# Performance work log

Measured on AMD Instinct MI355X. Metric: run time of the kernel, lower is better.

## Reference

```python
import jax, jax.numpy as jnp
import numpy as np

NEG_SLOPE = 0.01  # torch F.leaky_relu default

def _lrelu(x):
    return jax.nn.leaky_relu(x, NEG_SLOPE)

def setup_inputs() -> dict:
    key = jax.random.key(0)
    ks = jax.random.split(key, 24)
    B, N, E = 512, 20000, 640000
    n_enc_1, n_enc_2, n_z = 512, 256, 64
    n_dec_2, n_dec_1, hidden = 256, 512, 256
    p = lambda k, shp, fan: jax.random.normal(k, shp, jnp.float32) * (1.0 / np.sqrt(fan))
    return {
        "data": jax.random.normal(ks[0], (B, N), jnp.float32),
        "noise": jax.random.normal(ks[1], (B, N), jnp.float32),
        "edge_index": jax.random.randint(ks[2], (2, E), 0, N, jnp.int32),
        "w_gcn": jax.random.normal(ks[3], (), jnp.float32),
        "b_gcn": jax.random.normal(ks[4], (), jnp.float32) * 0.1,
        "enc1_w": p(ks[5], (N, n_enc_1), N), "enc1_b": p(ks[6], (n_enc_1,), N),
        "enc2_w": p(ks[7], (n_enc_1, n_enc_2), n_enc_1), "enc2_b": p(ks[8], (n_enc_2,), n_enc_1),
        "enc3_w": p(ks[9], (n_enc_2, n_z), n_enc_2), "enc3_b": p(ks[10], (n_z,), n_enc_2),
        "dec1_w": p(ks[11], (n_z, n_dec_2), n_z), "dec1_b": p(ks[12], (n_dec_2,), n_z),
        "dec2_w": p(ks[13], (n_dec_2, n_dec_1), n_dec_2), "dec2_b": p(ks[14], (n_dec_1,), n_dec_2),
        "dec3_w": p(ks[15], (n_dec_1, N), n_dec_1), "dec3_b": p(ks[16], (N,), n_dec_1),
        "disc1_w": p(ks[17], (n_z, hidden), n_z), "disc1_b": p(ks[18], (hidden,), n_z),
        "disc2_w": p(ks[19], (hidden, hidden), hidden), "disc2_b": p(ks[20], (hidden,), hidden),
        "disc3_w": p(ks[21], (hidden, 1), hidden), "disc3_b": p(ks[22], (1,), hidden),
    }

def _gcn_batched(x, edge_index, w_gcn, b_gcn):
    # x: [B, N] -> GCNConv(1,1, improved=True) applied per row, vectorized.
    B, N = x.shape
    src, dst = edge_index[0], edge_index[1]
    loop = jnp.arange(N, dtype=src.dtype)
    src_a = jnp.concatenate([src, loop])
    dst_a = jnp.concatenate([dst, loop])
    # improved=True: self-loop edge weight 2.0
    ew = jnp.concatenate([jnp.ones(src.shape[0], x.dtype), jnp.full((N,), 2.0, x.dtype)])
    deg = jax.ops.segment_sum(ew, dst_a, num_segments=N)
    dinv = jnp.where(deg > 0, jax.lax.rsqrt(deg), 0.0)
    norm = dinv[src_a] * ew * dinv[dst_a]  # [E+N]
    xl = x * w_gcn                         # lin (1x1 weight, no bias)
    msgs = xl[:, src_a] * norm[None, :]    # [B, E+N]
    agg = jnp.zeros_like(x).at[:, dst_a].add(msgs)
    return agg + b_gcn

def reference(data, noise, edge_index, w_gcn, b_gcn,
              enc1_w, enc1_b, enc2_w, enc2_b, enc3_w, enc3_b,
              dec1_w, dec1_b, dec2_w, dec2_b, dec3_w, dec3_b,
              disc1_w, disc1_b, disc2_w, disc2_b, disc3_w, disc3_b):
    x = data + noise * 0.1
    gcn_out = _lrelu(_gcn_batched(x, edge_index, w_gcn, b_gcn))  # [B, N]
    h1 = _lrelu(gcn_out @ enc1_w + enc1_b)
    h2 = _lrelu(h1 @ enc2_w + enc2_b)
    z = _lrelu(h2 @ enc3_w + enc3_b)
    d1 = _lrelu(z @ dec1_w + dec1_b)
    d2 = _lrelu(d1 @ dec2_w + dec2_b)
    dec_h3 = _lrelu(d2 @ dec3_w + dec3_b)
    g1 = _lrelu(z @ disc1_w + disc1_b)
    g2 = _lrelu(g1 @ disc2_w + disc2_b)
    d = jax.nn.sigmoid(g2 @ disc3_w + disc3_b)
    return (dec_h3, z, d)
```

## Files before the change

### kernel.cpp

```cpp
#include <hip/hip_runtime.h>
#include <hip/hip_bf16.h>


#define LRELU(v) ((v) > 0.f ? (v) : 0.01f * (v))

static constexpr int Bb = 512;
static constexpr int Nn = 20000;
static constexpr int Ee = 640000;
static constexpr int KPAD = 20480;
static constexpr int RSU = 36;
static constexpr int RSW = 18;

typedef __attribute__((ext_vector_type(8))) short short8;
typedef __attribute__((ext_vector_type(4))) short short4v;
typedef __attribute__((ext_vector_type(4))) float f32x4;

__device__ __forceinline__ ushort f2bf(float f) {
  uint u = __builtin_bit_cast(uint, f);
  u = u + 0x7FFFu + ((u >> 16) & 1u);
  return (ushort)(u >> 16);
}
__device__ __forceinline__ float bfLo(uint u) {
  return __builtin_bit_cast(float, u << 16);
}
__device__ __forceinline__ float bfHi(uint u) {
  return __builtin_bit_cast(float, u & 0xffff0000u);
}

__global__ void transpose_xs_k(const float* __restrict__ a, const float* __restrict__ nz,
                               const float* __restrict__ dinv, ushort* __restrict__ xs, int b0) {
  __shared__ ushort tile[64][65];
  int c0 = blockIdx.x * 64;
  int p = blockIdx.y;
  int chunk = p >> 1;
  int sub = (p & 1) * 64;
  int rbase = b0 + p * 64;
  for (int i = threadIdx.x; i < 64 * 64; i += 256) {
    int rr = i >> 6, cc = i & 63;
    int r = rbase + rr, c = c0 + cc;
    ushort v = 0;
    if (c < Nn) {
      size_t idx = (size_t)r * Nn + c;
      v = f2bf(dinv[c] * (a[idx] + 0.1f * nz[idx]));
    }
    tile[rr][cc] = v;
  }
  __syncthreads();
  for (int i = threadIdx.x; i < 64 * 64; i += 256) {
    int cc = i >> 6, rr = i & 63;
    int c = c0 + cc;
    if (c < Nn) xs[(size_t)chunk * Nn * 128 + (size_t)c * 128 + sub + rr] = tile[rr][cc];
  }
}

__global__ void hist_check_k(const int* __restrict__ src, const int* __restrict__ dst, int E,
                             int* __restrict__ cnt, int* __restrict__ flag) {
  int i = blockIdx.x * 256 + threadIdx.x;
  if (i < E) {
    int s = src[i], d = dst[i];
    if ((unsigned)s >= (unsigned)Nn || (unsigned)d >= (unsigned)Nn) {
      atomicExch(flag, 1);
    } else {
      atomicAdd(&cnt[d], 1);
    }
  }
}

__global__ void offs_k(const int* __restrict__ cnt, int* __restrict__ offs,
                       int* __restrict__ cursor, float* __restrict__ dinv,
                       int* __restrict__ bump) {
  int i = blockIdx.x * 256 + threadIdx.x;
  int l = threadIdx.x & 63;
  int v = (i < Nn) ? cnt[i] : 0;
  int x = v;
#pragma unroll
  for (int d = 1; d < 64; d <<= 1) {
    int t = __shfl_up(x, d);
    if (l >= d) x += t;
  }
  int total = __shfl(x, 63);
  int base = 0;
  if (l == 0) base = atomicAdd(bump, total);
  base = __shfl(base, 0);
  int excl = base + x - v;
  if (i < Nn) {
    offs[i] = excl;
    cursor[i] = excl;
    dinv[i] = rsqrtf(2.0f + (float)v);
  }
}

__global__ void scatter_k(const int* __restrict__ src, const int* __restrict__ dst, int E,
                          int* __restrict__ cursor, uint* __restrict__ eOff) {
  int i = blockIdx.x * 256 + threadIdx.x;
  if (i < E) {
    int s = src[i], d = dst[i];
    if ((unsigned)s >= (unsigned)Nn || (unsigned)d >= (unsigned)Nn) return;
    int p = atomicAdd(&cursor[d], 1);
    eOff[p] = (uint)s * 256u;
  }
}

__global__ __launch_bounds__(256) void spmm_chunk_k(
    const ushort* __restrict__ xs, const uint* __restrict__ eOff, const int* __restrict__ offs,
    const int* __restrict__ cnt, const float* __restrict__ dinv, const float* __restrict__ wg,
    const float* __restrict__ bg, ushort* __restrict__ gcnT, int NC) {
  __shared__ uint sIdx[4][64];
  int bid = blockIdx.x;
  int chunk = bid % NC;
  int ngrp = bid / NC;
  int wv = threadIdx.x >> 6, l = threadIdx.x & 63;
  int n = ngrp * 4 + wv;
  int o = offs[n], c = cnt[n];
  const char* base = (const char*)(xs + (size_t)chunk * Nn * 128) + l * 4;
  const uint* ep = eOff + o;
  uint su = *(const uint*)(base + (size_t)n * 256);
  float a00 = 2.0f * bfLo(su), a01 = 2.0f * bfHi(su);
  float a10 = 0.f, a11 = 0.f;

  for (int bi = 0; bi < c; bi += 64) {
    int rem = c - bi;
    if (rem > 64) rem = 64;
    sIdx[wv][l] = (l < rem) ? ep[bi + l] : 0u;
    int i = 0;
    for (; i + 8 <= rem; i += 8) {
      uint u[8];
#pragma unroll
      for (int j = 0; j < 8; ++j) u[j] = *(const uint*)(base + sIdx[wv][i + j]);
#pragma unroll
      for (int j = 0; j < 8; j += 2) {
        a00 += bfLo(u[j]);
        a01 += bfHi(u[j]);
        a10 += bfLo(u[j + 1]);
        a11 += bfHi(u[j + 1]);
      }
    }
    for (; i < rem; ++i) {
      uint u = *(const uint*)(base + sIdx[wv][i]);
      a00 += bfLo(u);
      a01 += bfHi(u);
    }
  }

  float wdn = wg[0] * dinv[n], bb = bg[0];
  float v0 = wdn * (a00 + a10) + bb;
  float v1 = wdn * (a01 + a11) + bb;
  v0 = LRELU(v0);
  v1 = LRELU(v1);
  uint pk = (uint)f2bf(v0) | ((uint)f2bf(v1) << 16);
  *(uint*)&gcnT[(size_t)chunk * KPAD * 128 + (size_t)n * 128 + 2 * l] = pk;
}

template <bool SPLITK>
__global__ __launch_bounds__(256) void mfma_gemm3(const ushort* __restrict__ AT, int lda, int pw,
                                                  size_t pstride, const float* __restrict__ B,
                                                  int ldb, int KB, int Nv, int iters,
                                                  float* __restrict__ C, int ldc,
                                                  const float* __restrict__ bias) {
  __shared__ ushort As[128 * RSU];
  __shared__ ushort Bs[128 * RSU];
  int n0 = blockIdx.x * 128, m0 = blockIdx.y * 128;
  int k0 = blockIdx.z * iters * 32;
  int tid = threadIdx.x;
  int kp = tid >> 4;
  int c8 = (tid & 15) * 8;
  int l = tid & 63, w = tid >> 6;
  int wr = w >> 1, wc = w & 1;
  int lrow = l & 15, lkg = l >> 4;
  const ushort* Ap = AT + (size_t)(m0 / pw) * pstride + (m0 % pw);
  int bcol = n0 + c8;
  bool bok = bcol < Nv;
  f32x4 acc[4][4] = {};

  uint4 pa0, pa1;
  float4 pb00, pb01, pb10, pb11;

#define GLOAD(KG)                                                                       \
  {                                                                                     \
    int kq = (KG) + 2 * kp;                                                             \
    pa0 = *(const uint4*)&Ap[(size_t)kq * lda + c8];                                    \
    pa1 = *(const uint4*)&Ap[(size_t)(kq + 1) * lda + c8];                              \
    pb00 = pb01 = pb10 = pb11 = float4{0.f, 0.f, 0.f, 0.f};                             \
    if (bok) {                                                                          \
      if (kq < KB) {                                                                    \
        const float4* bp = (const float4*)(B + (size_t)kq * ldb + bcol);                \
        pb00 = bp[0];                                                                   \
        pb01 = bp[1];                                                                   \
      }                                                                                 \
      if (kq + 1 < KB) {                                                                \
        const float4* bp = (const float4*)(B + (size_t)(kq + 1) * ldb + bcol);          \
        pb10 = bp[0];                                                                   \
        pb11 = bp[1];                                                                   \
      }                                                                                 \
    }                                                                                   \
  }

  GLOAD(k0);

  for (int kt = 0; kt < iters; ++kt) {
    uint wa[8], wb[8];
    wa[0] = (pa0.x & 0xffffu) | (pa1.x << 16);
    wa[1] = (pa0.x >> 16) | (pa1.x & 0xffff0000u);
    wa[2] = (pa0.y & 0xffffu) | (pa1.y << 16);
    wa[3] = (pa0.y >> 16) | (pa1.y & 0xffff0000u);
    wa[4] = (pa0.z & 0xffffu) | (pa1.z << 16);
    wa[5] = (pa0.z >> 16) | (pa1.z & 0xffff0000u);
    wa[6] = (pa0.w & 0xffffu) | (pa1.w << 16);
    wa[7] = (pa0.w >> 16) | (pa1.w & 0xffff0000u);
    wb[0] = (uint)f2bf(pb00.x) | ((uint)f2bf(pb10.x) << 16);
    wb[1] = (uint)f2bf(pb00.y) | ((uint)f2bf(pb10.y) << 16);
    wb[2] = (uint)f2bf(pb00.z) | ((uint)f2bf(pb10.z) << 16);
    wb[3] = (uint)f2bf(pb00.w) | ((uint)f2bf(pb10.w) << 16);
    wb[4] = (uint)f2bf(pb01.x) | ((uint)f2bf(pb11.x) << 16);
    wb[5] = (uint)f2bf(pb01.y) | ((uint)f2bf(pb11.y) << 16);
    wb[6] = (uint)f2bf(pb01.z) | ((uint)f2bf(pb11.z) << 16);
    wb[7] = (uint)f2bf(pb01.w) | ((uint)f2bf(pb11.w) << 16);
    __syncthreads();
    {
      uint* aw = (uint*)As;
      uint* bw = (uint*)Bs;
#pragma unroll
      for (int j = 0; j < 8; ++j) {
        aw[(c8 + j) * RSW + kp] = wa[j];
        bw[(c8 + j) * RSW + kp] = wb[j];
      }
    }
    __syncthreads();
    if (kt + 1 < iters) GLOAD(k0 + (kt + 1) * 32);
    short8 a[4], b[4];
#pragma unroll
    for (int mi = 0; mi < 4; ++mi) {
      int m = wr * 64 + mi * 16 + lrow;
      const short4v* p = (const short4v*)&As[m * RSU + lkg * 8];
      a[mi] = __builtin_shufflevector(p[0], p[1], 0, 1, 2, 3, 4, 5, 6, 7);
    }
#pragma unroll
    for (int nj = 0; nj < 4; ++nj) {
      int n = wc * 64 + nj * 16 + lrow;
      const short4v* p = (const short4v*)&Bs[n * RSU + lkg * 8];
      b[nj] = __builtin_shufflevector(p[0], p[1], 0, 1, 2, 3, 4, 5, 6, 7);
    }
#pragma unroll
    for (int mi = 0; mi < 4; ++mi)
#pragma unroll
      for (int nj = 0; nj < 4; ++nj)
        acc[mi][nj] = __builtin_amdgcn_mfma_f32_16x16x32_bf16(a[mi], b[nj], acc[mi][nj], 0, 0, 0);
  }
#undef GLOAD

#pragma unroll
  for (int mi = 0; mi < 4; ++mi)
#pragma unroll
    for (int nj = 0; nj < 4; ++nj)
#pragma unroll
      for (int r = 0; r < 4; ++r) {
        int row = m0 + wr * 64 + mi * 16 + lkg * 4 + r;
        int col = n0 + wc * 64 + nj * 16 + lrow;
        if (SPLITK) {
          atomicAdd(&C[(size_t)row * ldc + col], acc[mi][nj][r]);
        } else if (col < Nv) {
          float v = acc[mi][nj][r] + bias[col];
          C[(size_t)row * ldc + col] = LRELU(v);
        }
      }
}

__global__ __launch_bounds__(256) void tail2_k(
    const float* __restrict__ h1, const float* __restrict__ c1, const float* __restrict__ W2,
    const float* __restrict__ c2, const float* __restrict__ W3, const float* __restrict__ c3,
    const float* __restrict__ Wd1, const float* __restrict__ cd1, const float* __restrict__ Wd2,
    const float* __restrict__ cd2, const float* __restrict__ Wg1, const float* __restrict__ cg1,
    const float* __restrict__ Wg2, const float* __restrict__ cg2, const float* __restrict__ Wg3,
    const float* __restrict__ cg3, float* __restrict__ out_z, float* __restrict__ out_d,
    ushort* __restrict__ d2bfT, int BT, int b0) {
  __shared__ float s_h1[512];
  __shared__ float s_h2[256];
  __shared__ float s_z[64];
  __shared__ float s_d1[256];
  __shared__ float s_g1[256];
  __shared__ float s_g2[256];
  __shared__ float s_part[4][256];
  __shared__ float s_red[4];
  int rl = blockIdx.x;
  int rg = b0 + rl;
  int t = threadIdx.x;
  int w = t >> 6, l = t & 63;

  {
    float r0 = h1[(size_t)rl * 512 + t] + c1[t];
    float r1 = h1[(size_t)rl * 512 + t + 256] + c1[t + 256];
    s_h1[t] = LRELU(r0);
    s_h1[t + 256] = LRELU(r1);
  }
  __syncthreads();

  {
    int c4 = l * 4;
    float a0 = 0.f, a1 = 0.f, a2 = 0.f, a3 = 0.f;
#pragma unroll 8
    for (int k = w * 128; k < w * 128 + 128; ++k) {
      float4 wv = *(const float4*)&W2[(size_t)k * 256 + c4];
      float x = s_h1[k];
      a0 += x * wv.x; a1 += x * wv.y; a2 += x * wv.z; a3 += x * wv.w;
    }
    float4 pv = {a0, a1, a2, a3};
    *(float4*)&s_part[w][c4] = pv;
  }
  __syncthreads();
  s_h2[t] = LRELU(s_part[0][t] + s_part[1][t] + s_part[2][t] + s_part[3][t] + c2[t]);
  __syncthreads();

  {
    int c = t >> 2, p = t & 3;
    float a = 0.f;
#pragma unroll 8
    for (int k = p * 64; k < p * 64 + 64; ++k) a += s_h2[k] * W3[(size_t)k * 64 + c];
    s_part[p][c] = a;
  }
  __syncthreads();
  if (t < 64) {
    float v = s_part[0][t] + s_part[1][t] + s_part[2][t] + s_part[3][t] + c3[t];
    v = LRELU(v);
    s_z[t] = v;
    out_z[(size_t)rg * 64 + t] = v;
  }
  __syncthreads();

  {
    float a = 0.f;
#pragma unroll
    for (int k = 0; k < 64; ++k) a += s_z[k] * Wd1[(size_t)k * 256 + t];
    s_d1[t] = LRELU(a + cd1[t]);
  }
  {
    float a = 0.f;
#pragma unroll
    for (int k = 0; k < 64; ++k) a += s_z[k] * Wg1[(size_t)k * 256 + t];
    s_g1[t] = LRELU(a + cg1[t]);
  }
  __syncthreads();

  {
    int g = t & 127, p = t >> 7;
    int c4 = g * 4;
    float a0 = 0.f, a1 = 0.f, a2 = 0.f, a3 = 0.f;
#pragma unroll 8
    for (int k = p * 128; k < p * 128 + 128; ++k) {
      float4 wv = *(const float4*)&Wd2[(size_t)k * 512 + c4];
      float x = s_d1[k];
      a0 += x * wv.x; a1 += x * wv.y; a2 += x * wv.z; a3 += x * wv.w;
    }
    float* sp = &s_part[0][0];
    float4 pv = {a0, a1, a2, a3};
    *(float4*)&sp[p * 512 + c4] = pv;
  }
  __syncthreads();
  {
    const float* sp = &s_part[0][0];
#pragma unroll
    for (int cc = 0; cc < 2; ++cc) {
      int c = t + cc * 256;
      float v = sp[c] + sp[512 + c] + cd2[c];
      v = LRELU(v);
      d2bfT[(size_t)c * BT + rl] = f2bf(v);
    }
  }
  __syncthreads();

  {
    int c4 = l * 4;
    float a0 = 0.f, a1 = 0.f, a2 = 0.f, a3 = 0.f;
#pragma unroll 8
    for (int k = w * 64; k < w * 64 + 64; ++k) {
      float4 wv = *(const float4*)&Wg2[(size_t)k * 256 + c4];
      float x = s_g1[k];
      a0 += x * wv.x; a1 += x * wv.y; a2 += x * wv.z; a3 += x * wv.w;
    }
    float4 pv = {a0, a1, a2, a3};
    *(float4*)&s_part[w][c4] = pv;
  }
  __syncthreads();
  s_g2[t] = LRELU(s_part[0][t] + s_part[1][t] + s_part[2][t] + s_part[3][t] + cg2[t]);
  __syncthreads();

  {
    float p = s_g2[t] * Wg3[t];
#pragma unroll
    for (int o = 32; o > 0; o >>= 1) p += __shfl_down(p, o);
    if ((t & 63) == 0) s_red[t >> 6] = p;
    __syncthreads();
    if (t == 0) {
      float s = s_red[0] + s_red[1] + s_red[2] + s_red[3] + cg3[0];
      out_d[rg] = 1.f / (1.f + __expf(-s));
    }
  }
}

__global__ void sentinel_k(float* out, float val) { out[0] = val; }
__global__ void flag_sentinel_k(float* out, const int* flag) {
  if (*flag != 0) out[0] = 70000.0f;
}

extern "C" void kernel_launch(void* const* d_in, const int* in_sizes, int n_in,
                              void* d_out, int out_size, void* d_ws, size_t ws_size,
                              hipStream_t stream) {
  const float* data = (const float*)d_in[0];
  const float* noise = (const float*)d_in[1];
  const int* edge = (const int*)d_in[2];
  const int* esrc_in = edge;
  const int* edst_in = edge + Ee;
  const float* w_gcn = (const float*)d_in[3];
  const float* b_gcn = (const float*)d_in[4];
  const float* enc1_w = (const float*)d_in[5];
  const float* enc1_b = (const float*)d_in[6];
  const float* enc2_w = (const float*)d_in[7];
  const float* enc2_b = (const float*)d_in[8];
  const float* enc3_w = (const float*)d_in[9];
  const float* enc3_b = (const float*)d_in[10];
  const float* dec1_w = (const float*)d_in[11];
  const float* dec1_b = (const float*)d_in[12];
  const float* dec2_w = (const float*)d_in[13];
  const float* dec2_b = (const float*)d_in[14];
  const float* dec3_w = (const float*)d_in[15];
  const float* dec3_b = (const float*)d_in[16];
  const float* disc1_w = (const float*)d_in[17];
  const float* disc1_b = (const float*)d_in[18];
  const float* disc2_w = (const float*)d_in[19];
  const float* disc2_b = (const float*)d_in[20];
  const float* disc3_w = (const float*)d_in[21];
  const float* disc3_b = (const float*)d_in[22];

  int BT = 128;
  if (ws_size >= 48500000u) BT = 512;
  else if (ws_size >= 24392500u) BT = 256;
  int NC = BT / 128;
  if (NC < 1) NC = 1;

  char* w = (char*)d_ws;
  size_t o = 0;
  auto alloc = [&](size_t bytes) {
    size_t r = o;
    o = (o + bytes + 15) & ~(size_t)15;
    return r;
  };
  ushort* xs = (ushort*)(w + alloc((size_t)Nn * BT * 2));
  ushort* gcnT = (ushort*)(w + alloc((size_t)KPAD * BT * 2));
  float* h1 = (float*)(w + alloc((size_t)BT * 512 * 4));
  ushort* d2bfT = (ushort*)(w + alloc((size_t)512 * BT * 2));
  float* dinv = (float*)(w + alloc(Nn * 4));
  int* cnt = (int*)(w + alloc(Nn * 4));
  int* offs = (int*)(w + alloc(Nn * 4));
  int* cursor = (int*)(w + alloc(Nn * 4));
  uint* eOff = (uint*)(w + alloc(Ee * 4));
  int* flag = (int*)(w + alloc(16));

  float* outp = (float*)d_out;
  float* out_dec = outp;
  float* out_z = outp + (size_t)Bb * Nn;
  float* out_d = out_z + (size_t)Bb * 64;

  static const int expect_sizes[23] = {
      10240000, 10240000, 1280000, 1, 1,
      10240000, 512, 131072, 256, 16384, 64,
      16384, 256, 131072, 512, 10240000, 20000,
      16384, 256, 65536, 256, 256, 1};
  float host_sentinel = 0.f;
  if (n_in != 23) host_sentinel = 50000.f;
  else if (out_size != 10273280) host_sentinel = 80000.f;
  else {
    for (int i = 0; i < 23; ++i)
      if (in_sizes[i] != expect_sizes[i]) { host_sentinel = 100000.f + 1000.f * i; break; }
  }

  hipMemsetAsync(cnt, 0, Nn * sizeof(int), stream);
  hipMemsetAsync(flag, 0, 2 * sizeof(int), stream);
  hist_check_k<<<(Ee + 255) / 256, 256, 0, stream>>>(esrc_in, edst_in, Ee, cnt, flag);
  offs_k<<<(Nn + 255) / 256, 256, 0, stream>>>(cnt, offs, cursor, dinv, flag + 1);
  scatter_k<<<(Ee + 255) / 256, 256, 0, stream>>>(esrc_in, edst_in, Ee, cursor, eOff);
  hipMemsetAsync(gcnT, 0, (size_t)KPAD * BT * 2, stream);

  for (int b0 = 0; b0 < Bb; b0 += BT) {
    {
      dim3 g((Nn + 63) / 64, BT / 64);
      transpose_xs_k<<<g, 256, 0, stream>>>(data, noise, dinv, xs, b0);
    }
    spmm_chunk_k<<<(Nn / 4) * NC, 256, 0, stream>>>(xs, eOff, offs, cnt, dinv, w_gcn, b_gcn,
                                                    gcnT, NC);
    hipMemsetAsync(h1, 0, (size_t)BT * 512 * 4, stream);
    {
      dim3 g(512 / 128, BT / 128, 32);
      mfma_gemm3<true><<<g, 256, 0, stream>>>(gcnT, 128, 128, (size_t)KPAD * 128, enc1_w, 512,
                                              Nn, 512, 20, h1, 512, nullptr);
    }
    tail2_k<<<BT, 256, 0, stream>>>(h1, enc1_b, enc2_w, enc2_b, enc3_w, enc3_b, dec1_w, dec1_b,
                                    dec2_w, dec2_b, disc1_w, disc1_b, disc2_w, disc2_b, disc3_w,
                                    disc3_b, out_z, out_d, d2bfT, BT, b0);
    {
      dim3 g((Nn + 127) / 128, BT / 128, 1);
      mfma_gemm3<false><<<g, 256, 0, stream>>>(d2bfT, BT, BT, 0, dec3_w, Nn, 512, Nn, 16,
                                               out_dec + (size_t)b0 * Nn, Nn, dec3_b);
    }
  }

  flag_sentinel_k<<<1, 1, 0, stream>>>(out_dec, flag);
  if (host_sentinel != 0.f) sentinel_k<<<1, 1, 0, stream>>>(out_dec, host_sentinel);
}
```

Before: 297.8 us.

## Process full batch at once with 64-wide panels and fragment-layout dec3 GEMM

Drops the batch-chunk loop so the whole 512-row batch goes through one pass. Data is repacked into eight 64-row panels, and the SpMM now gives each half-wavefront its own node. The enc1 split-K GEMM uses more K splits. dec3 gets a new MFMA kernel that reads bf16 weights and activations pre-packed into fragment order straight from global memory, with no LDS staging. This trades a per-call bf16 conversion of dec3_w and a larger workspace requirement for fewer launches and better parallelism.

```diff
diff --git a/kernel.cpp b/kernel.cpp
--- a/kernel.cpp
+++ b/kernel.cpp
@@ -8,6 +8,7 @@
 static constexpr int Nn = 20000;
 static constexpr int Ee = 640000;
 static constexpr int KPAD = 20480;
+static constexpr int NPD = 20096;
 static constexpr int RSU = 36;
 static constexpr int RSW = 18;
 
@@ -28,13 +29,11 @@
 }
 
 __global__ void transpose_xs_k(const float* __restrict__ a, const float* __restrict__ nz,
-                               const float* __restrict__ dinv, ushort* __restrict__ xs, int b0) {
+                               const float* __restrict__ dinv, ushort* __restrict__ xs) {
   __shared__ ushort tile[64][65];
   int c0 = blockIdx.x * 64;
   int p = blockIdx.y;
-  int chunk = p >> 1;
-  int sub = (p & 1) * 64;
-  int rbase = b0 + p * 64;
+  int rbase = p * 64;
   for (int i = threadIdx.x; i < 64 * 64; i += 256) {
     int rr = i >> 6, cc = i & 63;
     int r = rbase + rr, c = c0 + cc;
@@ -49,7 +48,7 @@
   for (int i = threadIdx.x; i < 64 * 64; i += 256) {
     int cc = i >> 6, rr = i & 63;
     int c = c0 + cc;
-    if (c < Nn) xs[(size_t)chunk * Nn * 128 + (size_t)c * 128 + sub + rr] = tile[rr][cc];
+    if (c < Nn) xs[((size_t)p * Nn + c) * 64 + rr] = tile[rr][cc];
   }
 }
 
@@ -97,66 +96,63 @@
     int s = src[i], d = dst[i];
     if ((unsigned)s >= (unsigned)Nn || (unsigned)d >= (unsigned)Nn) return;
     int p = atomicAdd(&cursor[d], 1);
-    eOff[p] = (uint)s * 256u;
-  }
-}
-
-__global__ __launch_bounds__(256) void spmm_chunk_k(
+    eOff[p] = (uint)s * 128u;
+  }
+}
+
+__global__ __launch_bounds__(256) void spmm_p8_k(
     const ushort* __restrict__ xs, const uint* __restrict__ eOff, const int* __restrict__ offs,
     const int* __restrict__ cnt, const float* __restrict__ dinv, const float* __restrict__ wg,
-    const float* __restrict__ bg, ushort* __restrict__ gcnT, int NC) {
-  __shared__ uint sIdx[4][64];
+    const float* __restrict__ bg, ushort* __restrict__ gcnT) {
+  __shared__ uint sIdx[4][2][32];
   int bid = blockIdx.x;
-  int chunk = bid % NC;
-  int ngrp = bid / NC;
+  int panel = bid & 7;
   int wv = threadIdx.x >> 6, l = threadIdx.x & 63;
-  int n = ngrp * 4 + wv;
+  int h = l >> 5, q = l & 31;
+  int n = (bid >> 3) * 8 + wv * 2 + h;
   int o = offs[n], c = cnt[n];
-  const char* base = (const char*)(xs + (size_t)chunk * Nn * 128) + l * 4;
+  const char* base = (const char*)(xs + (size_t)panel * Nn * 64) + q * 4;
   const uint* ep = eOff + o;
-  uint su = *(const uint*)(base + (size_t)n * 256);
-  float a00 = 2.0f * bfLo(su), a01 = 2.0f * bfHi(su);
-  float a10 = 0.f, a11 = 0.f;
-
-  for (int bi = 0; bi < c; bi += 64) {
+  uint su = *(const uint*)(base + (size_t)n * 128);
+  float a0 = 2.0f * bfLo(su), a1 = 2.0f * bfHi(su);
+  float b0 = 0.f, b1 = 0.f;
+
+  for (int bi = 0; bi < c; bi += 32) {
     int rem = c - bi;
-    if (rem > 64) rem = 64;
-    sIdx[wv][l] = (l < rem) ? ep[bi + l] : 0u;
+    if (rem > 32) rem = 32;
+    sIdx[wv][h][q] = (q < rem) ? ep[bi + q] : 0u;
     int i = 0;
     for (; i + 8 <= rem; i += 8) {
       uint u[8];
 #pragma unroll
-      for (int j = 0; j < 8; ++j) u[j] = *(const uint*)(base + sIdx[wv][i + j]);
+      for (int j = 0; j < 8; ++j) u[j] = *(const uint*)(base + sIdx[wv][h][i + j]);
 #pragma unroll
       for (int j = 0; j < 8; j += 2) {
-        a00 += bfLo(u[j]);
-        a01 += bfHi(u[j]);
-        a10 += bfLo(u[j + 1]);
-        a11 += bfHi(u[j + 1]);
+        a0 += bfLo(u[j]);
+        a1 += bfHi(u[j]);
+        b0 += bfLo(u[j + 1]);
+        b1 += bfHi(u[j + 1]);
       }
     }
     for (; i < rem; ++i) {
-      uint u = *(const uint*)(base + sIdx[wv][i]);
-      a00 += bfLo(u);
-      a01 += bfHi(u);
+      uint u = *(const uint*)(base + sIdx[wv][h][i]);
+      a0 += bfLo(u);
+      a1 += bfHi(u);
     }
   }
 
   float wdn = wg[0] * dinv[n], bb = bg[0];
-  float v0 = wdn * (a00 + a10) + bb;
-  float v1 = wdn * (a01 + a11) + bb;
+  float v0 = wdn * (a0 + b0) + bb;
+  float v1 = wdn * (a1 + b1) + bb;
   v0 = LRELU(v0);
   v1 = LRELU(v1);
   uint pk = (uint)f2bf(v0) | ((uint)f2bf(v1) << 16);
-  *(uint*)&gcnT[(size_t)chunk * KPAD * 128 + (size_t)n * 128 + 2 * l] = pk;
-}
-
-template <bool SPLITK>
-__global__ __launch_bounds__(256) void mfma_gemm3(const ushort* __restrict__ AT, int lda, int pw,
-                                                  size_t pstride, const float* __restrict__ B,
-                                                  int ldb, int KB, int Nv, int iters,
-                                                  float* __restrict__ C, int ldc,
-                                                  const float* __restrict__ bias) {
+  *(uint*)&gcnT[((size_t)panel * KPAD + n) * 64 + 2 * q] = pk;
+}
+
+__global__ __launch_bounds__(256) void mfma_gemm3(const ushort* __restrict__ AT,
+                                                  const float* __restrict__ B, int ldb, int KB,
+                                                  int iters, float* __restrict__ C, int ldc) {
   __shared__ ushort As[128 * RSU];
   __shared__ ushort Bs[128 * RSU];
   int n0 = blockIdx.x * 128, m0 = blockIdx.y * 128;
@@ -167,32 +163,30 @@
   int l = tid & 63, w = tid >> 6;
   int wr = w >> 1, wc = w & 1;
   int lrow = l & 15, lkg = l >> 4;
-  const ushort* Ap = AT + (size_t)(m0 / pw) * pstride + (m0 % pw);
+  int gm = m0 + c8;
+  const ushort* Ap = AT + (size_t)(gm >> 6) * ((size_t)KPAD * 64) + (gm & 63);
   int bcol = n0 + c8;
-  bool bok = bcol < Nv;
   f32x4 acc[4][4] = {};
 
   uint4 pa0, pa1;
   float4 pb00, pb01, pb10, pb11;
 
-#define GLOAD(KG)                                                                       \
-  {                                                                                     \
-    int kq = (KG) + 2 * kp;                                                             \
-    pa0 = *(const uint4*)&Ap[(size_t)kq * lda + c8];                                    \
-    pa1 = *(const uint4*)&Ap[(size_t)(kq + 1) * lda + c8];                              \
-    pb00 = pb01 = pb10 = pb11 = float4{0.f, 0.f, 0.f, 0.f};                             \
-    if (bok) {                                                                          \
-      if (kq < KB) {                                                                    \
-        const float4* bp = (const float4*)(B + (size_t)kq * ldb + bcol);                \
-        pb00 = bp[0];                                                                   \
-        pb01 = bp[1];                                                                   \
-      }                                                                                 \
-      if (kq + 1 < KB) {                                                                \
-        const float4* bp = (const float4*)(B + (size_t)(kq + 1) * ldb + bcol);          \
-        pb10 = bp[0];                                                                   \
-        pb11 = bp[1];                                                                   \
-      }                                                                                 \
-    }                                                                                   \
+#define GLOAD(KG)                                                              \
+  {                                                                            \
+    int kq = (KG) + 2 * kp;                                                    \
+    pa0 = *(const uint4*)&Ap[(size_t)kq * 64];                                 \
+    pa1 = *(const uint4*)&Ap[(size_t)(kq + 1) * 64];                           \
+    pb00 = pb01 = pb10 = pb11 = float4{0.f, 0.f, 0.f, 0.f};                    \
+    if (kq < KB) {                                                             \
+      const float4* bp = (const float4*)(B + (size_t)kq * ldb + bcol);         \
+      pb00 = bp[0];                                                            \
+      pb01 = bp[1];                                                            \
+    }                                                                          \
+    if (kq + 1 < KB) {                                                         \
+      const float4* bp = (const float4*)(B + (size_t)(kq + 1) * ldb + bcol);   \
+      pb10 = bp[0];                                                            \
+      pb11 = bp[1];                                                            \
+    }                                                                          \
   }
 
   GLOAD(k0);
@@ -256,11 +250,68 @@
       for (int r = 0; r < 4; ++r) {
         int row = m0 + wr * 64 + mi * 16 + lkg * 4 + r;
         int col = n0 + wc * 64 + nj * 16 + lrow;
-        if (SPLITK) {
-          atomicAdd(&C[(size_t)row * ldc + col], acc[mi][nj][r]);
-        } else if (col < Nv) {
+        atomicAdd(&C[(size_t)row * ldc + col], acc[mi][nj][r]);
+      }
+}
+
+__global__ void conv_wf_k(const float* __restrict__ W, ushort* __restrict__ wf) {
+  int n = blockIdx.x * 256 + threadIdx.x;
+  int kb = blockIdx.y;
+  if (n >= NPD) return;
+  ushort v[8];
+#pragma unroll
+  for (int j = 0; j < 8; ++j)
+    v[j] = (n < Nn) ? f2bf(W[(size_t)(8 * kb + j) * Nn + n]) : (ushort)0;
+  uint4 pk;
+  pk.x = (uint)v[0] | ((uint)v[1] << 16);
+  pk.y = (uint)v[2] | ((uint)v[3] << 16);
+  pk.z = (uint)v[4] | ((uint)v[5] << 16);
+  pk.w = (uint)v[6] | ((uint)v[7] << 16);
+  *(uint4*)&wf[((size_t)kb * NPD + n) * 8] = pk;
+}
+
+__global__ __launch_bounds__(256) void fmg_dec3_k(const ushort* __restrict__ d2f,
+                                                  const ushort* __restrict__ wf,
+                                                  const float* __restrict__ bias,
+                                                  float* __restrict__ C) {
+  int n0 = blockIdx.x * 128, m0 = blockIdx.y * 128;
+  int l = threadIdx.x & 63, w = threadIdx.x >> 6;
+  int wr = w >> 1, wc = w & 1;
+  int lrow = l & 15, lkg = l >> 4;
+  f32x4 acc[4][4] = {};
+
+#pragma unroll 4
+  for (int ks = 0; ks < 16; ++ks) {
+    int kb = ks * 4 + lkg;
+    short8 a[4], b[4];
+#pragma unroll
+    for (int mi = 0; mi < 4; ++mi) {
+      int m = m0 + wr * 64 + mi * 16 + lrow;
+      a[mi] = *(const short8*)&d2f[((size_t)kb * 512 + m) * 8];
+    }
+#pragma unroll
+    for (int nj = 0; nj < 4; ++nj) {
+      int n = n0 + wc * 64 + nj * 16 + lrow;
+      b[nj] = *(const short8*)&wf[((size_t)kb * NPD + n) * 8];
+    }
+#pragma unroll
+    for (int mi = 0; mi < 4; ++mi)
+#pragma unroll
+      for (int nj = 0; nj < 4; ++nj)
+        acc[mi][nj] = __builtin_amdgcn_mfma_f32_16x16x32_bf16(a[mi], b[nj], acc[mi][nj], 0, 0, 0);
+  }
+
+#pragma unroll
+  for (int mi = 0; mi < 4; ++mi)
+#pragma unroll
+    for (int nj = 0; nj < 4; ++nj)
+#pragma unroll
+      for (int r = 0; r < 4; ++r) {
+        int row = m0 + wr * 64 + mi * 16 + lkg * 4 + r;
+        int col = n0 + wc * 64 + nj * 16 + lrow;
+        if (col < Nn) {
           float v = acc[mi][nj][r] + bias[col];
-          C[(size_t)row * ldc + col] = LRELU(v);
+          C[(size_t)row * Nn + col] = LRELU(v);
         }
       }
 }
@@ -272,7 +323,7 @@
     const float* __restrict__ cd2, const float* __restrict__ Wg1, const float* __restrict__ cg1,
     const float* __restrict__ Wg2, const float* __restrict__ cg2, const float* __restrict__ Wg3,
     const float* __restrict__ cg3, float* __restrict__ out_z, float* __restrict__ out_d,
-    ushort* __restrict__ d2bfT, int BT, int b0) {
+    ushort* __restrict__ d2f) {
   __shared__ float s_h1[512];
   __shared__ float s_h2[256];
   __shared__ float s_z[64];
@@ -282,7 +333,6 @@
   __shared__ float s_part[4][256];
   __shared__ float s_red[4];
   int rl = blockIdx.x;
-  int rg = b0 + rl;
   int t = threadIdx.x;
   int w = t >> 6, l = t & 63;
 
@@ -322,7 +372,7 @@
     float v = s_part[0][t] + s_part[1][t] + s_part[2][t] + s_part[3][t] + c3[t];
     v = LRELU(v);
     s_z[t] = v;
-    out_z[(size_t)rg * 64 + t] = v;
+    out_z[(size_t)rl * 64 + t] = v;
   }
   __syncthreads();
 
@@ -362,7 +412,7 @@
       int c = t + cc * 256;
       float v = sp[c] + sp[512 + c] + cd2[c];
       v = LRELU(v);
-      d2bfT[(size_t)c * BT + rl] = f2bf(v);
+      d2f[((size_t)(c >> 3) * 512 + rl) * 8 + (c & 7)] = f2bf(v);
     }
   }
   __syncthreads();
@@ -391,7 +441,7 @@
     __syncthreads();
     if (t == 0) {
       float s = s_red[0] + s_red[1] + s_red[2] + s_red[3] + cg3[0];
-      out_d[rg] = 1.f / (1.f + __expf(-s));
+      out_d[rl] = 1.f / (1.f + __expf(-s));
     }
   }
 }
@@ -430,12 +480,6 @@
   const float* disc3_w = (const float*)d_in[21];
   const float* disc3_b = (const float*)d_in[22];
 
-  int BT = 128;
-  if (ws_size >= 48500000u) BT = 512;
-  else if (ws_size >= 24392500u) BT = 256;
-  int NC = BT / 128;
-  if (NC < 1) NC = 1;
-
   char* w = (char*)d_ws;
   size_t o = 0;
   auto alloc = [&](size_t bytes) {
@@ -443,10 +487,12 @@
     o = (o + bytes + 15) & ~(size_t)15;
     return r;
   };
-  ushort* xs = (ushort*)(w + alloc((size_t)Nn * BT * 2));
-  ushort* gcnT = (ushort*)(w + alloc((size_t)KPAD * BT * 2));
-  float* h1 = (float*)(w + alloc((size_t)BT * 512 * 4));
-  ushort* d2bfT = (ushort*)(w + alloc((size_t)512 * BT * 2));
+  size_t r1 = alloc((size_t)64 * NPD * 8 * 2);
+  ushort* xs = (ushort*)(w + r1);
+  ushort* wf = (ushort*)(w + r1);
+  ushort* gcnT = (ushort*)(w + alloc((size_t)8 * KPAD * 64 * 2));
+  float* h1 = (float*)(w + alloc(512 * 512 * 4));
+  ushort* d2f = (ushort*)(w + alloc((size_t)64 * 512 * 8 * 2));
   float* dinv = (float*)(w + alloc(Nn * 4));
   int* cnt = (int*)(w + alloc(Nn * 4));
   int* offs = (int*)(w + alloc(Nn * 4));
@@ -467,6 +513,7 @@
   float host_sentinel = 0.f;
   if (n_in != 23) host_sentinel = 50000.f;
   else if (out_size != 10273280) host_sentinel = 80000.f;
+  else if (ws_size < 46200000u) host_sentinel = 60000.f;
   else {
     for (int i = 0; i < 23; ++i)
       if (in_sizes[i] != expect_sizes[i]) { host_sentinel = 100000.f + 1000.f * i; break; }
@@ -477,29 +524,28 @@
   hist_check_k<<<(Ee + 255) / 256, 256, 0, stream>>>(esrc_in, edst_in, Ee, cnt, flag);
   offs_k<<<(Nn + 255) / 256, 256, 0, stream>>>(cnt, offs, cursor, dinv, flag + 1);
   scatter_k<<<(Ee + 255) / 256, 256, 0, stream>>>(esrc_in, edst_in, Ee, cursor, eOff);
-  hipMemsetAsync(gcnT, 0, (size_t)KPAD * BT * 2, stream);
-
-  for (int b0 = 0; b0 < Bb; b0 += BT) {
-    {
-      dim3 g((Nn + 63) / 64, BT / 64);
-      transpose_xs_k<<<g, 256, 0, stream>>>(data, noise, dinv, xs, b0);
-    }
-    spmm_chunk_k<<<(Nn / 4) * NC, 256, 0, stream>>>(xs, eOff, offs, cnt, dinv, w_gcn, b_gcn,
-                                                    gcnT, NC);
-    hipMemsetAsync(h1, 0, (size_t)BT * 512 * 4, stream);
-    {
-      dim3 g(512 / 128, BT / 128, 32);
-      mfma_gemm3<true><<<g, 256, 0, stream>>>(gcnT, 128, 128, (size_t)KPAD * 128, enc1_w, 512,
-                                              Nn, 512, 20, h1, 512, nullptr);
-    }
-    tail2_k<<<BT, 256, 0, stream>>>(h1, enc1_b, enc2_w, enc2_b, enc3_w, enc3_b, dec1_w, dec1_b,
-                                    dec2_w, dec2_b, disc1_w, disc1_b, disc2_w, disc2_b, disc3_w,
-                                    disc3_b, out_z, out_d, d2bfT, BT, b0);
-    {
-      dim3 g((Nn + 127) / 128, BT / 128, 1);
-      mfma_gemm3<false><<<g, 256, 0, stream>>>(d2bfT, BT, BT, 0, dec3_w, Nn, 512, Nn, 16,
-                                               out_dec + (size_t)b0 * Nn, Nn, dec3_b);
-    }
+  hipMemsetAsync(gcnT, 0, (size_t)8 * KPAD * 64 * 2, stream);
+
+  {
+    dim3 g((Nn + 63) / 64, 8);
+    transpose_xs_k<<<g, 256, 0, stream>>>(data, noise, dinv, xs);
+  }
+  spmm_p8_k<<<(Nn / 8) * 8, 256, 0, stream>>>(xs, eOff, offs, cnt, dinv, w_gcn, b_gcn, gcnT);
+  hipMemsetAsync(h1, 0, 512 * 512 * 4, stream);
+  {
+    dim3 g(512 / 128, 512 / 128, 64);
+    mfma_gemm3<<<g, 256, 0, stream>>>(gcnT, enc1_w, 512, Nn, 10, h1, 512);
+  }
+  tail2_k<<<Bb, 256, 0, stream>>>(h1, enc1_b, enc2_w, enc2_b, enc3_w, enc3_b, dec1_w, dec1_b,
+                                  dec2_w, dec2_b, disc1_w, disc1_b, disc2_w, disc2_b, disc3_w,
+                                  disc3_b, out_z, out_d, d2f);
+  {
+    dim3 g((NPD + 255) / 256, 64);
+    conv_wf_k<<<g, 256, 0, stream>>>(dec3_w, wf);
+  }
+  {
+    dim3 g(NPD / 128, 512 / 128);
+    fmg_dec3_k<<<g, 256, 0, stream>>>(d2f, wf, dec3_b, out_dec);
   }
 
   flag_sentinel_k<<<1, 1, 0, stream>>>(out_dec, flag);
```

New measurement: 308.9 us. +3.7%, slower.
